# Optimization experiments

Measured on AMD Instinct MI355X. Metric: run time of the kernel, lower is better.

The kernel has to match this reference:

```python
import jax, jax.numpy as jnp
from jax import lax
import numpy as np

BLOCK_SIZE = 11   # cv2 blockSize (odd)
CONSTANT = 2.0    # cv2 C
MAXVAL = 255.0


def _box_mean(x, k):
    """Local k x k mean with BORDER_REPLICATE, matching cv2 ADAPTIVE_THRESH_MEAN_C.
    x: [N,H,W,1] float32. Separable 1-D box filters for efficiency."""
    pad = k // 2
    xp = jnp.pad(x, ((0, 0), (pad, pad), (pad, pad), (0, 0)), mode='edge')
    kh = jnp.full((k, 1, 1, 1), 1.0 / k, dtype=x.dtype)  # HWIO
    kw = jnp.full((1, k, 1, 1), 1.0 / k, dtype=x.dtype)
    dn = ('NHWC', 'HWIO', 'NHWC')
    y = lax.conv_general_dilated(xp, kh, (1, 1), 'VALID', dimension_numbers=dn)
    y = lax.conv_general_dilated(y, kw, (1, 1), 'VALID', dimension_numbers=dn)
    return y  # [N,H,W,1]


def setup_inputs() -> dict:
    key = jax.random.key(0)
    # grayscale pixel intensities in [0, 255]
    x = jax.random.uniform(key, (128, 512, 512, 1), dtype=jnp.float32) * 255.0
    return {"x": x}


def reference(x):
    # cv2.adaptiveThreshold(..., ADAPTIVE_THRESH_MEAN_C, THRESH_BINARY_INV, blockSize, C):
    #   T(x,y) = mean_{kxk}(src) - C
    #   dst = 0 if src > T else maxValue
    thresh = _box_mean(x, BLOCK_SIZE) - CONSTANT
    out = jnp.where(x > thresh, jnp.float32(0.0), jnp.float32(MAXVAL))
    return out
```

## Files before the change

kernel.cpp:

```cpp
#include <hip/hip_runtime.h>


constexpr int W   = 512;
constexpr int H   = 512;
constexpr int PAD = 5;
constexpr int KS  = 11;
constexpr int CPT = 8;
constexpr int TPB = 256;
constexpr int WPB = 4;
constexpr int RPB = 16;
constexpr int STRIPS = H / RPB;

typedef float f32x4 __attribute__((ext_vector_type(4)));

__global__ __launch_bounds__(TPB)
void AdaptiveThresholding_57904749085171_kernel(const float* __restrict__ x,
                                                float* __restrict__ out)
{
    const int l     = (int)threadIdx.x & 63;
    const int wv_id = (int)threadIdx.x >> 6;
    const int strip = (int)blockIdx.x * WPB + wv_id;
    const int img   = strip / STRIPS;
    const int y0    = (strip % STRIPS) * RPB;
    const size_t ioff = (size_t)img * (size_t)(W * H);
    const float* __restrict__ xi = x + ioff;
    float* __restrict__ oi = out + ioff;
    const int cbase = l * CPT;
    const float wv = (float)(1.0 / 11.0);

    float ring[KS][CPT];

    #pragma unroll
    for (int j = 0; j < KS - 1; ++j) {
        int row = y0 - PAD + j;
        row = row < 0 ? 0 : (row >= H ? H - 1 : row);
        const f32x4* p = (const f32x4*)(xi + (size_t)row * W + cbase);
        const f32x4 a = p[0], b = p[1];
        #pragma unroll
        for (int i = 0; i < 4; ++i) { ring[j][i] = a[i]; ring[j][4 + i] = b[i]; }
    }

    #pragma unroll
    for (int k = 0; k < RPB; ++k) {
        {
            int row = y0 + PAD + k;
            row = row >= H ? H - 1 : row;
            const f32x4* p = (const f32x4*)(xi + (size_t)row * W + cbase);
            const f32x4 a = p[0], b = p[1];
            #pragma unroll
            for (int i = 0; i < 4; ++i) {
                ring[(10 + k) % KS][i]     = a[i];
                ring[(10 + k) % KS][4 + i] = b[i];
            }
        }

        float a[CPT];
        #pragma unroll
        for (int i = 0; i < CPT; ++i) {
            float s = 0.0f;
            #pragma unroll
            for (int d = 0; d < KS; ++d) s = fmaf(ring[(k + d) % KS][i], wv, s);
            a[i] = s;
        }

        float z[CPT + 2 * PAD];
        #pragma unroll
        for (int q = 0; q < PAD; ++q) {
            const float vL = __shfl(a[3 + q], l - 1, 64);
            z[q] = (l == 0) ? a[0] : vL;
        }
        #pragma unroll
        for (int i = 0; i < CPT; ++i) z[PAD + i] = a[i];
        #pragma unroll
        for (int q = 0; q < PAD; ++q) {
            const float vR = __shfl(a[q], l + 1, 64);
            z[PAD + CPT + q] = (l == 63) ? a[7] : vR;
        }

        float o[CPT];
        #pragma unroll
        for (int i = 0; i < CPT; ++i) {
            float m = 0.0f;
            #pragma unroll
            for (int d = 0; d < KS; ++d) m = fmaf(z[i + d], wv, m);
            const float xv = ring[(k + PAD) % KS][i];
            o[i] = (xv > m - 2.0f) ? 0.0f : 255.0f;
        }

        f32x4 o0, o1;
        #pragma unroll
        for (int i = 0; i < 4; ++i) { o0[i] = o[i]; o1[i] = o[4 + i]; }
        f32x4* op = (f32x4*)(oi + (size_t)(y0 + k) * W + cbase);
        op[0] = o0;
        op[1] = o1;
    }
}

extern "C" void kernel_launch(void* const* d_in, const int* in_sizes, int n_in,
                              void* d_out, int out_size, void* d_ws, size_t ws_size,
                              hipStream_t stream)
{
    const float* x = (const float*)d_in[0];
    float* out = (float*)d_out;
    const int n_imgs = in_sizes[0] / (W * H);
    const int n_strips = n_imgs * STRIPS;

    dim3 grid(n_strips / WPB);
    dim3 block(TPB);
    AdaptiveThresholding_57904749085171_kernel<<<grid, block, 0, stream>>>(x, out);
}
```

Measured before the change: 62.30 us.

## Prefetch rows two ahead, swizzle blocks across XCDs, raise occupancy hint

Loads for input rows are issued two iterations ahead into a small double buffer, so global load latency overlaps the vertical and horizontal sum work. Block indices are remapped so each XCD processes a contiguous range of strips, which is meant to improve L2 reuse of the halo rows shared by neighbouring strips. The launch bounds now request 4 blocks per CU, and the z staging array is replaced with compile-time selection among the left halo, centre and right halo values. The prefetch adds register pressure, and the occupancy hint may force spills.

```diff
diff --git a/kernel.cpp b/kernel.cpp
--- a/kernel.cpp
+++ b/kernel.cpp
@@ -10,16 +10,22 @@
 constexpr int WPB = 4;
 constexpr int RPB = 16;
 constexpr int STRIPS = H / RPB;
+constexpr int NXCD = 8;
 
 typedef float f32x4 __attribute__((ext_vector_type(4)));
 
-__global__ __launch_bounds__(TPB)
+__global__ __launch_bounds__(TPB, 4)
 void AdaptiveThresholding_57904749085171_kernel(const float* __restrict__ x,
                                                 float* __restrict__ out)
 {
     const int l     = (int)threadIdx.x & 63;
     const int wv_id = (int)threadIdx.x >> 6;
-    const int strip = (int)blockIdx.x * WPB + wv_id;
+
+    const int cpx = (int)gridDim.x / NXCD;
+    const int bid = (int)blockIdx.x;
+    const int swz = (bid % NXCD) * cpx + bid / NXCD;
+
+    const int strip = swz * WPB + wv_id;
     const int img   = strip / STRIPS;
     const int y0    = (strip % STRIPS) * RPB;
     const size_t ioff = (size_t)img * (size_t)(W * H);
@@ -29,6 +35,7 @@
     const float wv = (float)(1.0 / 11.0);
 
     float ring[KS][CPT];
+    float pf[2][CPT];
 
     #pragma unroll
     for (int j = 0; j < KS - 1; ++j) {
@@ -39,19 +46,28 @@
         #pragma unroll
         for (int i = 0; i < 4; ++i) { ring[j][i] = a[i]; ring[j][4 + i] = b[i]; }
     }
+    #pragma unroll
+    for (int k = 0; k < 2; ++k) {
+        int row = y0 + PAD + k;
+        row = row >= H ? H - 1 : row;
+        const f32x4* p = (const f32x4*)(xi + (size_t)row * W + cbase);
+        const f32x4 a = p[0], b = p[1];
+        #pragma unroll
+        for (int i = 0; i < 4; ++i) { pf[k][i] = a[i]; pf[k][4 + i] = b[i]; }
+    }
 
     #pragma unroll
     for (int k = 0; k < RPB; ++k) {
-        {
-            int row = y0 + PAD + k;
+        #pragma unroll
+        for (int i = 0; i < CPT; ++i) ring[(10 + k) % KS][i] = pf[k & 1][i];
+
+        if (k + 2 < RPB) {
+            int row = y0 + PAD + k + 2;
             row = row >= H ? H - 1 : row;
             const f32x4* p = (const f32x4*)(xi + (size_t)row * W + cbase);
             const f32x4 a = p[0], b = p[1];
             #pragma unroll
-            for (int i = 0; i < 4; ++i) {
-                ring[(10 + k) % KS][i]     = a[i];
-                ring[(10 + k) % KS][4 + i] = b[i];
-            }
+            for (int i = 0; i < 4; ++i) { pf[k & 1][i] = a[i]; pf[k & 1][4 + i] = b[i]; }
         }
 
         float a[CPT];
@@ -63,18 +79,13 @@
             a[i] = s;
         }
 
-        float z[CPT + 2 * PAD];
+        float zl[PAD], zr[PAD];
         #pragma unroll
         for (int q = 0; q < PAD; ++q) {
             const float vL = __shfl(a[3 + q], l - 1, 64);
-            z[q] = (l == 0) ? a[0] : vL;
-        }
-        #pragma unroll
-        for (int i = 0; i < CPT; ++i) z[PAD + i] = a[i];
-        #pragma unroll
-        for (int q = 0; q < PAD; ++q) {
+            zl[q] = (l == 0) ? a[0] : vL;
             const float vR = __shfl(a[q], l + 1, 64);
-            z[PAD + CPT + q] = (l == 63) ? a[7] : vR;
+            zr[q] = (l == 63) ? a[7] : vR;
         }
 
         float o[CPT];
@@ -82,7 +93,13 @@
         for (int i = 0; i < CPT; ++i) {
             float m = 0.0f;
             #pragma unroll
-            for (int d = 0; d < KS; ++d) m = fmaf(z[i + d], wv, m);
+            for (int d = 0; d < KS; ++d) {
+                const int j = i + d;
+                const float zv = (j < PAD) ? zl[j]
+                               : (j < PAD + CPT) ? a[j - PAD]
+                               : zr[j - PAD - CPT];
+                m = fmaf(zv, wv, m);
+            }
             const float xv = ring[(k + PAD) % KS][i];
             o[i] = (xv > m - 2.0f) ? 0.0f : 255.0f;
         }
```

Result: slower. 178.7 us (+186.8%).
